# Kernel optimization log

Hardware: AMD Instinct MI355X
Metric: run time of the kernel (lower is better)

Reference implementation:

```python
import jax, jax.numpy as jnp
import numpy as np

H, C = 3, 64  # heads, per-head channels
NEG_SLOPE = 0.2

def setup_inputs() -> dict:
    key = jax.random.key(0)
    ks = jax.random.split(key, 8)
    B, N, D, E = 2, 50000, 128, 800000
    h = jax.random.normal(ks[0], (B, N, D), dtype=jnp.float32)
    edge_index = jax.random.randint(ks[1], (2, E), 0, N, dtype=jnp.int64)
    s = 1.0 / np.sqrt(D)
    W = jax.random.normal(ks[2], (D, H * C), dtype=jnp.float32) * s
    a_src = jax.random.normal(ks[3], (H, C), dtype=jnp.float32) * (1.0 / np.sqrt(C))
    a_dst = jax.random.normal(ks[4], (H, C), dtype=jnp.float32) * (1.0 / np.sqrt(C))
    bias = jnp.zeros((H * C,), dtype=jnp.float32)
    Wo = jax.random.normal(ks[5], (H * C, 1), dtype=jnp.float32) * (1.0 / np.sqrt(H * C))
    bo = jnp.zeros((1,), dtype=jnp.float32)
    return {"h": h, "edge_index": edge_index, "W": W, "a_src": a_src,
            "a_dst": a_dst, "bias": bias, "Wo": Wo, "bo": bo}

def _gat_single(h_b, src, dst, N, W, a_src, a_dst, bias):
    # h_b: [N, D] -> x: [N, H, C]
    x = (h_b @ W).reshape(-1, H, C)
    alpha_s = jnp.einsum('nhc,hc->nh', x, a_src)  # [N, H]
    alpha_d = jnp.einsum('nhc,hc->nh', x, a_dst)  # [N, H]
    e = alpha_s[src] + alpha_d[dst]               # [E', H]
    e = jnp.where(e > 0, e, NEG_SLOPE * e)        # leaky_relu(0.2)
    # segment softmax over edges grouped by destination node
    emax = jax.ops.segment_max(e, dst, num_segments=N)          # [N, H]
    p = jnp.exp(e - emax[dst])
    denom = jax.ops.segment_sum(p, dst, num_segments=N)         # [N, H]
    att = p / (denom[dst] + 1e-16)                               # [E', H]
    out = jax.ops.segment_sum(att[:, :, None] * x[src], dst, num_segments=N)  # [N,H,C]
    return out.reshape(-1, H * C) + bias

def reference(h, edge_index, W, a_src, a_dst, bias, Wo, bo):
    B, N, D = h.shape
    # PyG GATConv default: add self loops
    loops = jnp.arange(N, dtype=edge_index.dtype)
    src = jnp.concatenate([edge_index[0], loops])
    dst = jnp.concatenate([edge_index[1], loops])
    gat = jax.vmap(lambda hb: _gat_single(hb, src, dst, N, W, a_src, a_dst, bias))(h)
    gat = jax.nn.elu(gat)            # [B, N, H*C]; dropout inactive (eval)
    logits = gat @ Wo + bo           # [B, N, 1]
    return logits
```

## Files before the change

kernel.cpp:

```cpp
#include <hip/hip_runtime.h>
#include <hip/hip_bf16.h>
#include <math.h>

typedef __hip_bfloat16 bf16;
typedef __attribute__((ext_vector_type(8))) short short8;
typedef __attribute__((ext_vector_type(4))) float f32x4;

#define HC 192
#define DIN 128
#define NEG_SLOPE 0.2f
#define LCH 128
#define GN 4

static inline int cdiv(int a, int b){ return (a + b - 1) / b; }

__device__ inline short f2bf(float f){
  __hip_bfloat16 b = __float2bfloat16(f);
  return __builtin_bit_cast(short, b);
}
__device__ inline float loadf(const void* p, size_t i, int fm){
  return fm ? __bfloat162float(((const bf16*)p)[i]) : ((const float*)p)[i];
}
__device__ inline int eload(const void* p, long long i, int em){
  return em ? (int)(((const long long*)p)[i]) : ((const int*)p)[i];
}

__device__ inline int detect_fm(const unsigned* __restrict__ hw){
  unsigned w = hw[threadIdx.x & 63];
  unsigned expo = (w >> 7) & 0xFF;
  unsigned long long m = __ballot(expo >= 100 && expo <= 135);
  return __popcll(m) > 32;
}
__device__ inline int detect_em(const unsigned* __restrict__ ew){
  unsigned long long m = __ballot(ew[2*(threadIdx.x & 63) + 1] != 0);
  return __popcll(m) < 32;
}

__global__ void k_repack(const void* __restrict__ W, const void* __restrict__ a_src,
    const void* __restrict__ a_dst, const void* __restrict__ bias,
    const void* __restrict__ Wo, const void* __restrict__ bo,
    const unsigned* __restrict__ hw, bf16* __restrict__ Wt,
    float* __restrict__ asf, float* __restrict__ adf, float* __restrict__ biasf,
    float* __restrict__ Wof, float* __restrict__ bof){
  int fm = detect_fm(hw);
  int idx = blockIdx.x * 256 + threadIdx.x;
  if (idx < DIN * HC){
    int d = idx / HC, j = idx - d * HC;
    Wt[j * DIN + d] = __float2bfloat16(loadf(W, idx, fm));
  }
  if (idx < HC){
    asf[idx]   = loadf(a_src, idx, fm);
    adf[idx]   = loadf(a_dst, idx, fm);
    biasf[idx] = loadf(bias, idx, fm);
    Wof[idx]   = loadf(Wo, idx, fm);
  }
  if (idx == 0) bof[0] = loadf(bo, 0, fm);
}

__global__ __launch_bounds__(256) void k_gemm(const void* __restrict__ h,
    const bf16* __restrict__ Wt, bf16* __restrict__ x,
    const float* __restrict__ asf, const float* __restrict__ adf,
    float* __restrict__ asp, float* __restrict__ adp, int M, int N){
  int fm   = detect_fm((const unsigned*)h);
  int tid  = threadIdx.x;
  int w    = tid >> 6;
  int lane = tid & 63;
  int r16  = lane & 15;
  int quad = lane >> 4;
  __shared__ short ldsW[HC * 136];
  for (int c = tid; c < HC * 16; c += 256){
    int row = c >> 4, kg = c & 15;
    *(short8*)&ldsW[row * 136 + kg * 8] = *(const short8*)(Wt + row * DIN + kg * 8);
  }
  __syncthreads();

  int row  = blockIdx.x * 64 + w * 16 + r16;
  int lrow = min(row, M - 1);
  f32x4 acc[12];
  #pragma unroll
  for (int i = 0; i < 12; i++) acc[i] = (f32x4){0.f,0.f,0.f,0.f};
  size_t abase = (size_t)lrow * DIN + quad * 8;
  #pragma unroll
  for (int kb = 0; kb < 4; kb++){
    short8 af;
    if (fm == 0){
      const float* hf = (const float*)h + abase + kb * 32;
      float4 a = *(const float4*)hf;
      float4 b = *(const float4*)(hf + 4);
      af[0]=f2bf(a.x); af[1]=f2bf(a.y); af[2]=f2bf(a.z); af[3]=f2bf(a.w);
      af[4]=f2bf(b.x); af[5]=f2bf(b.y); af[6]=f2bf(b.z); af[7]=f2bf(b.w);
    } else {
      af = *(const short8*)((const bf16*)h + abase + kb * 32);
    }
    #pragma unroll
    for (int nt = 0; nt < 12; nt++){
      short8 bf_ = *(const short8*)&ldsW[(nt*16 + r16) * 136 + kb * 32 + quad * 8];
      acc[nt] = __builtin_amdgcn_mfma_f32_16x16x32_bf16(af, bf_, acc[nt], 0,0,0);
    }
  }
  int rbase = blockIdx.x * 64 + w * 16 + quad * 4;
  #pragma unroll
  for (int nt = 0; nt < 12; nt++){
    #pragma unroll
    for (int r = 0; r < 4; r++){
      int rr = rbase + r;
      if (rr < M) x[(size_t)rr * HC + nt*16 + r16] = __float2bfloat16(acc[nt][r]);
    }
  }
  float asv[12], adv[12];
  #pragma unroll
  for (int nt = 0; nt < 12; nt++){
    int col = (nt >> 2) * 64 + (nt & 3) * 16 + r16;
    asv[nt] = asf[col];
    adv[nt] = adf[col];
  }
  #pragma unroll
  for (int hh = 0; hh < 3; hh++){
    #pragma unroll
    for (int r = 0; r < 4; r++){
      float vs = acc[4*hh+0][r]*asv[4*hh+0] + acc[4*hh+1][r]*asv[4*hh+1]
               + acc[4*hh+2][r]*asv[4*hh+2] + acc[4*hh+3][r]*asv[4*hh+3];
      float vd = acc[4*hh+0][r]*adv[4*hh+0] + acc[4*hh+1][r]*adv[4*hh+1]
               + acc[4*hh+2][r]*adv[4*hh+2] + acc[4*hh+3][r]*adv[4*hh+3];
      #pragma unroll
      for (int off = 8; off; off >>= 1){
        vs += __shfl_down(vs, off, 16);
        vd += __shfl_down(vd, off, 16);
      }
      if (r16 == 0){
        int rr = rbase + r;
        if (rr < M){
          int b = rr >= N;
          int node = rr - b * N;
          asp[(size_t)node*8 + b*3 + hh] = vs;
          adp[(size_t)node*8 + b*3 + hh] = vd;
        }
      }
    }
  }
}

__global__ void k_hist(const void* __restrict__ ei, int E, int N, int* counts){
  int em = detect_em((const unsigned*)ei);
  int idx = blockIdx.x * 256 + threadIdx.x;
  if (idx >= E + N) return;
  int d = (idx < E) ? eload(ei, (long long)E + idx, em) : (idx - E);
  if ((unsigned)d < (unsigned)N) atomicAdd(&counts[d], 1);
}

__global__ __launch_bounds__(256) void k_scanA(const int* __restrict__ counts,
    int* __restrict__ partial, int* __restrict__ bsums, int N){
  __shared__ int s[256];
  int t = threadIdx.x, idx = blockIdx.x * 256 + t;
  int v = (idx < N) ? counts[idx] : 0;
  s[t] = v; __syncthreads();
  for (int o = 1; o < 256; o <<= 1){
    int u = (t >= o) ? s[t - o] : 0;
    __syncthreads();
    s[t] += u;
    __syncthreads();
  }
  if (idx < N) partial[idx] = s[t] - v;
  if (t == 255) bsums[blockIdx.x] = s[255];
}

__global__ __launch_bounds__(256) void k_scanC(const int* __restrict__ partial,
    const int* __restrict__ bsums, int* __restrict__ row_ptr,
    int* __restrict__ cursor, int N, int nb){
  __shared__ int s[256];
  int t = threadIdx.x;
  int v = (t < nb) ? bsums[t] : 0;
  s[t] = v; __syncthreads();
  for (int o = 1; o < 256; o <<= 1){
    int u = (t >= o) ? s[t - o] : 0;
    __syncthreads();
    s[t] += u;
    __syncthreads();
  }
  int excl = s[t] - v;
  __syncthreads();
  s[t] = excl;
  __syncthreads();
  int idx = blockIdx.x * 256 + t;
  int boff = s[blockIdx.x];
  if (idx < N){
    int val = partial[idx] + boff;
    row_ptr[idx] = val;
    cursor[idx]  = val;
  } else if (idx == N){
    row_ptr[N] = s[nb-1] + bsums[nb-1];
  }
}

__global__ void k_scatter(const void* __restrict__ ei, int E, int N,
    int* cursor, int* __restrict__ esorted){
  int em = detect_em((const unsigned*)ei);
  int idx = blockIdx.x * 256 + threadIdx.x;
  if (idx >= E + N) return;
  int s, d;
  if (idx < E){
    s = eload(ei, idx, em);
    d = eload(ei, (long long)E + idx, em);
  } else { s = d = idx - E; }
  if ((unsigned)d >= (unsigned)N) return;
  if ((unsigned)s >= (unsigned)N) s = 0;
  int p = atomicAdd(&cursor[d], 1);
  esorted[p] = s;
}

__global__ __launch_bounds__(192) void k_gat(const bf16* __restrict__ x,
    const int* __restrict__ esorted, const int* __restrict__ row_ptr,
    const float* __restrict__ asp, const float* __restrict__ adp,
    const float* __restrict__ biasf, const float* __restrict__ Wof,
    const float* __restrict__ bof, float* __restrict__ out, int N){
  int blk  = blockIdx.x;
  int t    = threadIdx.x;
  int node = t / 48;
  int u    = t - node * 48;
  int b    = u >= 24;
  int c8   = u - b * 24;
  int hh   = c8 >> 3;
  __shared__ int   rp[GN + 1];
  __shared__ float ldsD[GN * 8];
  __shared__ float ldsP[LCH * 8];
  __shared__ float red[192];
  if (t < GN + 1) rp[t] = row_ptr[GN*blk + t];
  if (t >= 8 && t < 8 + GN*2){
    int i = t - 8;
    ((float4*)ldsD)[i] = ((const float4*)adp)[(size_t)(GN*blk + (i>>1))*2 + (i&1)];
  }
  __syncthreads();
  int start = rp[node], end = rp[node + 1];
  int base0 = rp[0], cend = rp[GN];
  const ushort* xb = (const ushort*)x + (size_t)b * N * HC + c8 * 8;
  int pidx = b*3 + hh;
  float acc[8];
  #pragma unroll
  for (int k = 0; k < 8; k++) acc[k] = 0.f;
  float den = 0.f;
  for (int cb = base0; cb < cend; cb += LCH){
    int cnt = min(LCH, cend - cb);
    __syncthreads();
    if (t < cnt){
      int gi = cb + t;
      int s  = esorted[gi];
      int dn = (gi >= rp[1]) + (gi >= rp[2]) + (gi >= rp[3]);
      float4 A0 = ((const float4*)asp)[(size_t)s*2];
      float4 A1 = ((const float4*)asp)[(size_t)s*2 + 1];
      const float* D = &ldsD[dn*8];
      float e0 = A0.x + D[0], e1 = A0.y + D[1], e2 = A0.z + D[2];
      float e3 = A0.w + D[3], e4 = A1.x + D[4], e5 = A1.y + D[5];
      e0 = e0 > 0.f ? e0 : NEG_SLOPE*e0;  e1 = e1 > 0.f ? e1 : NEG_SLOPE*e1;
      e2 = e2 > 0.f ? e2 : NEG_SLOPE*e2;  e3 = e3 > 0.f ? e3 : NEG_SLOPE*e3;
      e4 = e4 > 0.f ? e4 : NEG_SLOPE*e4;  e5 = e5 > 0.f ? e5 : NEG_SLOPE*e5;
      float* P = &ldsP[t*8];
      P[0] = __expf(e0); P[1] = __expf(e1); P[2] = __expf(e2);
      P[3] = __expf(e3); P[4] = __expf(e4); P[5] = __expf(e5);
      P[6] = __int_as_float(s);
    }
    __syncthreads();
    int i0 = max(start, cb), i1 = min(end, cb + cnt);
    #pragma unroll 4
    for (int i = i0; i < i1; i++){
      int rec = i - cb;
      float p = ldsP[rec*8 + pidx];
      int s   = __float_as_int(ldsP[rec*8 + 6]);
      uint4 q = *(const uint4*)(xb + (size_t)s * HC);
      den += p;
      acc[0] = fmaf(p, __uint_as_float(q.x << 16),         acc[0]);
      acc[1] = fmaf(p, __uint_as_float(q.x & 0xffff0000u), acc[1]);
      acc[2] = fmaf(p, __uint_as_float(q.y << 16),         acc[2]);
      acc[3] = fmaf(p, __uint_as_float(q.y & 0xffff0000u), acc[3]);
      acc[4] = fmaf(p, __uint_as_float(q.z << 16),         acc[4]);
      acc[5] = fmaf(p, __uint_as_float(q.z & 0xffff0000u), acc[5]);
      acc[6] = fmaf(p, __uint_as_float(q.w << 16),         acc[6]);
      acc[7] = fmaf(p, __uint_as_float(q.w & 0xffff0000u), acc[7]);
    }
  }
  float inv = 1.f / (den + 1e-16f);
  float4 bi0 = ((const float4*)biasf)[c8*2], bi1 = ((const float4*)biasf)[c8*2+1];
  float4 w0  = ((const float4*)Wof)[c8*2],  w1  = ((const float4*)Wof)[c8*2+1];
  float r = 0.f;
  {
    float v;
    v = acc[0]*inv + bi0.x; v = v > 0.f ? v : expm1f(v); r += v * w0.x;
    v = acc[1]*inv + bi0.y; v = v > 0.f ? v : expm1f(v); r += v * w0.y;
    v = acc[2]*inv + bi0.z; v = v > 0.f ? v : expm1f(v); r += v * w0.z;
    v = acc[3]*inv + bi0.w; v = v > 0.f ? v : expm1f(v); r += v * w0.w;
    v = acc[4]*inv + bi1.x; v = v > 0.f ? v : expm1f(v); r += v * w1.x;
    v = acc[5]*inv + bi1.y; v = v > 0.f ? v : expm1f(v); r += v * w1.y;
    v = acc[6]*inv + bi1.z; v = v > 0.f ? v : expm1f(v); r += v * w1.z;
    v = acc[7]*inv + bi1.w; v = v > 0.f ? v : expm1f(v); r += v * w1.w;
  }
  red[t] = r;
  __syncthreads();
  if (t < 64){
    int g = t >> 3, l = t & 7;
    float v = red[g*24 + l] + red[g*24 + 8 + l] + red[g*24 + 16 + l];
    v += __shfl_down(v, 4, 8);
    v += __shfl_down(v, 2, 8);
    v += __shfl_down(v, 1, 8);
    if (l == 0){
      int nd = GN*blk + (g >> 1);
      int bb = g & 1;
      out[(size_t)bb * N + nd] = v + bof[0];
    }
  }
}

extern "C" void kernel_launch(void* const* d_in, const int* in_sizes, int n_in,
                              void* d_out, int out_size, void* d_ws, size_t ws_size,
                              hipStream_t stream){
  const void* h     = d_in[0];
  const void* ei    = d_in[1];
  const void* W     = d_in[2];
  const void* a_src = d_in[3];
  const void* a_dst = d_in[4];
  const void* bias  = d_in[5];
  const void* Wo    = d_in[6];
  const void* bo    = d_in[7];
  float* out = (float*)d_out;

  const int M    = in_sizes[0] / DIN;
  const int N    = M / 2;
  const int E    = in_sizes[1] / 2;
  const int Etot = E + N;

  char* ws = (char*)d_ws;
  size_t off = 0;
  auto alloc = [&](size_t bytes) -> void* {
    void* p = ws + off;
    off = (off + bytes + 511) & ~(size_t)511;
    return p;
  };
  bf16*  x       = (bf16*) alloc((size_t)M * HC * sizeof(bf16));
  float* asp     = (float*)alloc((size_t)N * 8 * sizeof(float));
  float* adp     = (float*)alloc((size_t)N * 8 * sizeof(float));
  int*   counts  = (int*)  alloc((size_t)N * sizeof(int));
  int*   partial = (int*)  alloc((size_t)N * sizeof(int));
  int*   row_ptr = (int*)  alloc((size_t)(N + 1) * sizeof(int));
  int*   cursor  = (int*)  alloc((size_t)N * sizeof(int));
  int*   bsums   = (int*)  alloc(256 * sizeof(int));
  int*   esorted = (int*)  alloc((size_t)Etot * sizeof(int));
  bf16*  Wt      = (bf16*) alloc((size_t)DIN * HC * sizeof(bf16));
  float* asf     = (float*)alloc(HC * sizeof(float));
  float* adf     = (float*)alloc(HC * sizeof(float));
  float* biasf   = (float*)alloc(HC * sizeof(float));
  float* Wof     = (float*)alloc(HC * sizeof(float));
  float* bof     = (float*)alloc(16 * sizeof(float));
  (void)ws_size; (void)n_in; (void)out_size;

  hipMemsetAsync(counts, 0, (size_t)N * sizeof(int), stream);

  k_repack<<<cdiv(DIN * HC, 256), 256, 0, stream>>>(W, a_src, a_dst, bias, Wo, bo,
      (const unsigned*)h, Wt, asf, adf, biasf, Wof, bof);
  k_gemm<<<cdiv(M, 64), 256, 0, stream>>>(h, Wt, x, asf, adf, asp, adp, M, N);
  k_hist<<<cdiv(Etot, 256), 256, 0, stream>>>(ei, E, N, counts);
  int nb = cdiv(N, 256);
  k_scanA<<<nb, 256, 0, stream>>>(counts, partial, bsums, N);
  k_scanC<<<cdiv(N + 1, 256), 256, 0, stream>>>(partial, bsums, row_ptr, cursor, N, nb);
  k_scatter<<<cdiv(Etot, 256), 256, 0, stream>>>(ei, E, N, cursor, esorted);
  k_gat<<<N / GN, 192, 0, stream>>>(x, esorted, row_ptr, asp, adp, biasf, Wof, bof, out, N);
}
```

Measured before the change: 311.5 us.

## Precompute per-edge attention exps in a separate kernel with fp16 packed records

Moves the per-edge attention logit, leaky-relu and exp computation out of the aggregation kernel into a new pass over the sorted edges. The scatter now stores (src,dst) pairs, and the new pass writes 16-byte records holding six fp16 exp values plus the source index. The aggregation kernel then only streams these records into shared memory before gathering features. This costs an extra launch, an extra round trip through memory for edge records, and lower precision (fp16) for the unnormalised exp values, which could overflow for large logits.

```diff
diff --git a/kernel.cpp b/kernel.cpp
--- a/kernel.cpp
+++ b/kernel.cpp
@@ -23,6 +23,15 @@
 }
 __device__ inline int eload(const void* p, long long i, int em){
   return em ? (int)(((const long long*)p)[i]) : ((const int*)p)[i];
+}
+__device__ inline unsigned pack2h(float a, float b){
+  unsigned short ha = __builtin_bit_cast(unsigned short, (_Float16)a);
+  unsigned short hb = __builtin_bit_cast(unsigned short, (_Float16)b);
+  return (unsigned)ha | ((unsigned)hb << 16);
+}
+__device__ inline float unph(unsigned w, int hi){
+  unsigned short hs = hi ? (unsigned short)(w >> 16) : (unsigned short)(w & 0xffff);
+  return (float)__builtin_bit_cast(_Float16, hs);
 }
 
 __device__ inline int detect_fm(const unsigned* __restrict__ hw){
@@ -193,7 +202,7 @@
 }
 
 __global__ void k_scatter(const void* __restrict__ ei, int E, int N,
-    int* cursor, int* __restrict__ esorted){
+    int* cursor, int2* __restrict__ esd){
   int em = detect_em((const unsigned*)ei);
   int idx = blockIdx.x * 256 + threadIdx.x;
   if (idx >= E + N) return;
@@ -205,12 +214,34 @@
   if ((unsigned)d >= (unsigned)N) return;
   if ((unsigned)s >= (unsigned)N) s = 0;
   int p = atomicAdd(&cursor[d], 1);
-  esorted[p] = s;
+  esd[p] = make_int2(s, d);
+}
+
+__global__ __launch_bounds__(256) void k_pe(const int2* __restrict__ esd,
+    const float* __restrict__ asp, const float* __restrict__ adp,
+    uint4* __restrict__ pe, int Etot){
+  int j = blockIdx.x * 256 + threadIdx.x;
+  if (j >= Etot) return;
+  int2 sd = esd[j];
+  float4 A0 = ((const float4*)asp)[(size_t)sd.x*2];
+  float4 A1 = ((const float4*)asp)[(size_t)sd.x*2 + 1];
+  float4 D0 = ((const float4*)adp)[(size_t)sd.y*2];
+  float4 D1 = ((const float4*)adp)[(size_t)sd.y*2 + 1];
+  float e0 = A0.x + D0.x, e1 = A0.y + D0.y, e2 = A0.z + D0.z;
+  float e3 = A0.w + D0.w, e4 = A1.x + D1.x, e5 = A1.y + D1.y;
+  e0 = e0 > 0.f ? e0 : NEG_SLOPE*e0;  e1 = e1 > 0.f ? e1 : NEG_SLOPE*e1;
+  e2 = e2 > 0.f ? e2 : NEG_SLOPE*e2;  e3 = e3 > 0.f ? e3 : NEG_SLOPE*e3;
+  e4 = e4 > 0.f ? e4 : NEG_SLOPE*e4;  e5 = e5 > 0.f ? e5 : NEG_SLOPE*e5;
+  uint4 rec;
+  rec.x = pack2h(__expf(e0), __expf(e1));
+  rec.y = pack2h(__expf(e2), __expf(e3));
+  rec.z = pack2h(__expf(e4), __expf(e5));
+  rec.w = (unsigned)sd.x;
+  pe[j] = rec;
 }
 
 __global__ __launch_bounds__(192) void k_gat(const bf16* __restrict__ x,
-    const int* __restrict__ esorted, const int* __restrict__ row_ptr,
-    const float* __restrict__ asp, const float* __restrict__ adp,
+    const uint4* __restrict__ pe, const int* __restrict__ row_ptr,
     const float* __restrict__ biasf, const float* __restrict__ Wof,
     const float* __restrict__ bof, float* __restrict__ out, int N){
   int blk  = blockIdx.x;
@@ -221,19 +252,16 @@
   int c8   = u - b * 24;
   int hh   = c8 >> 3;
   __shared__ int   rp[GN + 1];
-  __shared__ float ldsD[GN * 8];
-  __shared__ float ldsP[LCH * 8];
+  __shared__ uint4 ldsR[LCH];
   __shared__ float red[192];
   if (t < GN + 1) rp[t] = row_ptr[GN*blk + t];
-  if (t >= 8 && t < 8 + GN*2){
-    int i = t - 8;
-    ((float4*)ldsD)[i] = ((const float4*)adp)[(size_t)(GN*blk + (i>>1))*2 + (i&1)];
-  }
   __syncthreads();
   int start = rp[node], end = rp[node + 1];
   int base0 = rp[0], cend = rp[GN];
   const ushort* xb = (const ushort*)x + (size_t)b * N * HC + c8 * 8;
   int pidx = b*3 + hh;
+  int pw_i = pidx >> 1, pw_h = pidx & 1;
+  unsigned* ldsU = (unsigned*)ldsR;
   float acc[8];
   #pragma unroll
   for (int k = 0; k < 8; k++) acc[k] = 0.f;
@@ -241,30 +269,14 @@
   for (int cb = base0; cb < cend; cb += LCH){
     int cnt = min(LCH, cend - cb);
     __syncthreads();
-    if (t < cnt){
-      int gi = cb + t;
-      int s  = esorted[gi];
-      int dn = (gi >= rp[1]) + (gi >= rp[2]) + (gi >= rp[3]);
-      float4 A0 = ((const float4*)asp)[(size_t)s*2];
-      float4 A1 = ((const float4*)asp)[(size_t)s*2 + 1];
-      const float* D = &ldsD[dn*8];
-      float e0 = A0.x + D[0], e1 = A0.y + D[1], e2 = A0.z + D[2];
-      float e3 = A0.w + D[3], e4 = A1.x + D[4], e5 = A1.y + D[5];
-      e0 = e0 > 0.f ? e0 : NEG_SLOPE*e0;  e1 = e1 > 0.f ? e1 : NEG_SLOPE*e1;
-      e2 = e2 > 0.f ? e2 : NEG_SLOPE*e2;  e3 = e3 > 0.f ? e3 : NEG_SLOPE*e3;
-      e4 = e4 > 0.f ? e4 : NEG_SLOPE*e4;  e5 = e5 > 0.f ? e5 : NEG_SLOPE*e5;
-      float* P = &ldsP[t*8];
-      P[0] = __expf(e0); P[1] = __expf(e1); P[2] = __expf(e2);
-      P[3] = __expf(e3); P[4] = __expf(e4); P[5] = __expf(e5);
-      P[6] = __int_as_float(s);
-    }
+    for (int j = t; j < cnt; j += 192) ldsR[j] = pe[(size_t)cb + j];
     __syncthreads();
     int i0 = max(start, cb), i1 = min(end, cb + cnt);
     #pragma unroll 4
     for (int i = i0; i < i1; i++){
       int rec = i - cb;
-      float p = ldsP[rec*8 + pidx];
-      int s   = __float_as_int(ldsP[rec*8 + 6]);
+      float p = unph(ldsU[rec*4 + pw_i], pw_h);
+      int s   = (int)ldsU[rec*4 + 3];
       uint4 q = *(const uint4*)(xb + (size_t)s * HC);
       den += p;
       acc[0] = fmaf(p, __uint_as_float(q.x << 16),         acc[0]);
@@ -341,7 +353,8 @@
   int*   row_ptr = (int*)  alloc((size_t)(N + 1) * sizeof(int));
   int*   cursor  = (int*)  alloc((size_t)N * sizeof(int));
   int*   bsums   = (int*)  alloc(256 * sizeof(int));
-  int*   esorted = (int*)  alloc((size_t)Etot * sizeof(int));
+  int2*  esd     = (int2*) alloc((size_t)Etot * sizeof(int2));
+  uint4* pe      = (uint4*)alloc((size_t)Etot * sizeof(uint4));
   bf16*  Wt      = (bf16*) alloc((size_t)DIN * HC * sizeof(bf16));
   float* asf     = (float*)alloc(HC * sizeof(float));
   float* adf     = (float*)alloc(HC * sizeof(float));
@@ -359,6 +372,7 @@
   int nb = cdiv(N, 256);
   k_scanA<<<nb, 256, 0, stream>>>(counts, partial, bsums, N);
   k_scanC<<<cdiv(N + 1, 256), 256, 0, stream>>>(partial, bsums, row_ptr, cursor, N, nb);
-  k_scatter<<<cdiv(Etot, 256), 256, 0, stream>>>(ei, E, N, cursor, esorted);
-  k_gat<<<N / GN, 192, 0, stream>>>(x, esorted, row_ptr, asp, adp, biasf, Wof, bof, out, N);
-}
+  k_scatter<<<cdiv(Etot, 256), 256, 0, stream>>>(ei, E, N, cursor, esd);
+  k_pe<<<cdiv(Etot, 256), 256, 0, stream>>>(esd, asp, adp, pe, Etot);
+  k_gat<<<N / GN, 192, 0, stream>>>(x, pe, row_ptr, biasf, Wof, bof, out, N);
+}
```

New measurement: 315.1 us. No clear change (+1.2%).
